# Performance work log

Measured on AMD Instinct MI355X. Metric: run time of the kernel, lower is better.

The kernel has to match this reference:

```python
import jax, jax.numpy as jnp
import numpy as np

SEQ_LEN = 720
PRED_LEN = 720
PERIOD = 24
EMB = 64
P_IN = SEQ_LEN // PERIOD            # 30
P_OUT = -(-PRED_LEN // PERIOD)      # 30 (ceil)
FREQ = EMB // 2 + 1                 # 33
DOM = (SEQ_LEN // PERIOD + 1) * 2 + 10  # 72
RATIO = PRED_LEN / SEQ_LEN          # 1.0


def _clin(z, Wr, Wi, br, bi):
    # complex nn.Linear over last dim: z @ W.T + b
    W = Wr + 1j * Wi
    b = br + 1j * bi
    return jnp.einsum('...i,oi->...o', z, W) + b


def _forward(x, freq_Wr, freq_Wi, freq_br, freq_bi, WP_W, WP_b, W_pos,
             mix1_Wr, mix1_Wi, mix1_br, mix1_bi,
             fmix_Wr, fmix_Wi, fmix_br, fmix_bi,
             proj_Wr, proj_Wi, proj_br, proj_bi,
             head_W, head_b):
    B, T, N = x.shape
    # ---- low-frequency branch ----
    low = jnp.fft.rfft(x, axis=1)[:, :DOM, :]               # [B, DOM, N] complex
    low = jnp.swapaxes(low, 1, 2)                           # [B, N, DOM]
    low = _clin(low, freq_Wr, freq_Wi, freq_br, freq_bi)    # [B, N, DOM_out]
    low = jnp.swapaxes(low, 1, 2)                           # [B, DOM_out, N]
    out_bins = PRED_LEN // 2 + 1
    low = jnp.pad(low, ((0, 0), (0, out_bins - low.shape[1]), (0, 0)))
    low_xy = jnp.fft.irfft(low, n=PRED_LEN, axis=1) * RATIO  # [B, PRED_LEN, N]

    # ---- period branch (single fixed period 24; SEQ_LEN % 24 == 0) ----
    xk = jnp.swapaxes(x, 1, 2).reshape(B, N, P_IN, PERIOD)  # unfold(size=step=24)
    xk = jnp.einsum('bnpi,oi->bnpo', xk, WP_W) + WP_b       # [B,N,P_IN,EMB]
    pf = jnp.fft.rfft(xk, axis=-1) + W_pos                  # [B,N,P_IN,FREQ] (W_pos real -> real part)
    pf = jnp.swapaxes(pf, -1, -2)                           # [B,N,FREQ,P_IN]
    o = _clin(pf, mix1_Wr, mix1_Wi, mix1_br, mix1_bi) + pf
    o = jnp.swapaxes(_clin(jnp.swapaxes(o, -1, -2), fmix_Wr, fmix_Wi, fmix_br, fmix_bi), -1, -2) + o
    o = _clin(o, proj_Wr, proj_Wi, proj_br, proj_bi)        # [B,N,FREQ,P_OUT]
    o = jnp.swapaxes(o, -1, -2)                             # [B,N,P_OUT,FREQ]
    pp = jnp.fft.irfft(o, n=EMB, axis=-1).reshape(B, N, P_OUT * EMB)
    pred = jnp.einsum('bnf,of->bno', pp, head_W) + head_b   # [B,N,PRED_LEN]
    pred = jnp.swapaxes(pred, 1, 2)                         # [B,PRED_LEN,N]
    return 0.7 * pred + 0.3 * low_xy


def setup_inputs() -> dict:
    B, N = 128, 128
    ks = jax.random.split(jax.random.key(0), 22)
    f32 = jnp.float32
    def w(k, shape, s=0.05):
        return jax.random.normal(k, shape, dtype=f32) * s
    return {
        'x': jax.random.normal(ks[0], (B, SEQ_LEN, N), dtype=f32),
        'freq_Wr': w(ks[1], (DOM, DOM)), 'freq_Wi': w(ks[2], (DOM, DOM)),
        'freq_br': w(ks[3], (DOM,)), 'freq_bi': w(ks[4], (DOM,)),
        'WP_W': w(ks[5], (EMB, PERIOD)), 'WP_b': w(ks[6], (EMB,)),
        'W_pos': jax.random.uniform(ks[7], (B, N, P_IN, FREQ), dtype=f32, minval=-0.02, maxval=0.02),
        'mix1_Wr': w(ks[8], (P_IN, P_IN)), 'mix1_Wi': w(ks[9], (P_IN, P_IN)),
        'mix1_br': w(ks[10], (P_IN,)), 'mix1_bi': w(ks[11], (P_IN,)),
        'fmix_Wr': w(ks[12], (FREQ, FREQ)), 'fmix_Wi': w(ks[13], (FREQ, FREQ)),
        'fmix_br': w(ks[14], (FREQ,)), 'fmix_bi': w(ks[15], (FREQ,)),
        'proj_Wr': w(ks[16], (P_OUT, P_IN)), 'proj_Wi': w(ks[17], (P_OUT, P_IN)),
        'proj_br': w(ks[18], (P_OUT,)), 'proj_bi': w(ks[19], (P_OUT,)),
        'head_W': w(ks[20], (PRED_LEN, P_OUT * EMB)), 'head_b': w(ks[21], (PRED_LEN,)),
    }


def reference(x, freq_Wr, freq_Wi, freq_br, freq_bi, WP_W, WP_b, W_pos,
              mix1_Wr, mix1_Wi, mix1_br, mix1_bi,
              fmix_Wr, fmix_Wi, fmix_br, fmix_bi,
              proj_Wr, proj_Wi, proj_br, proj_bi,
              head_W, head_b):
    return _forward(x, freq_Wr, freq_Wi, freq_br, freq_bi, WP_W, WP_b, W_pos,
                    mix1_Wr, mix1_Wi, mix1_br, mix1_bi,
                    fmix_Wr, fmix_Wi, fmix_br, fmix_bi,
                    proj_Wr, proj_Wi, proj_br, proj_bi,
                    head_W, head_b)
```

## Files before the change

kernel.cpp:

```cpp
#include <hip/hip_runtime.h>
#include <hip/hip_bf16.h>
#include <math.h>

#define SEQ 720
#define NCH 128
#define BATCH 128
#define BN 16384
#define DOM 72
#define PIN 30
#define POUT 30
#define FRQ 33
#define EMB 64
#define PER 24
#define KW 990
#define KP 1728
#define MT 768
#define PI_F 3.14159265358979323846f

typedef float2 cf;
typedef __attribute__((ext_vector_type(8))) short short8v;
__device__ __forceinline__ cf cmac(cf acc, cf a, cf b){
  acc.x += a.x*b.x - a.y*b.y; acc.y += a.x*b.y + a.y*b.x; return acc;
}
__device__ __forceinline__ short b2s(float f){
  __hip_bfloat16 h = __float2bfloat16(f);
  return *reinterpret_cast<short*>(&h);
}

__global__ __launch_bounds__(512) void fused_pre(
                         const float* __restrict__ WPW, const float* __restrict__ WPb,
                         const float* __restrict__ m1r, const float* __restrict__ m1i,
                         const float* __restrict__ m1br, const float* __restrict__ m1bi,
                         const float* __restrict__ fxr, const float* __restrict__ fxi,
                         const float* __restrict__ fxbr, const float* __restrict__ fxbi,
                         const float* __restrict__ pjr, const float* __restrict__ pji,
                         const float* __restrict__ pjbr, const float* __restrict__ pjbi,
                         const float* __restrict__ fqr, const float* __restrict__ fqi,
                         const float* __restrict__ x, const float* __restrict__ Wp,
                         cf* C, cf* PM, cf* M2, cf* o3b,
                         float* __restrict__ A1r, float* __restrict__ A1i,
                         __hip_bfloat16* __restrict__ Abig)
{
  __shared__ double arena_d[5900];
  char* smem = (char*)arena_d;
  int tid = threadIdx.x;
  int blk = blockIdx.x;

  if (blk < DOM){
    cf* tbl  = (cf*)(smem);
    cf* wrow = (cf*)(smem + 5760);
    int k = blk;
    for (int m=tid;m<720;m+=512){ float s,c; sincosf(-2.f*PI_F*(float)m/720.f,&s,&c); tbl[m]=make_float2(c,s); }
    for (int j=tid;j<DOM;j+=512) wrow[j]=make_float2(fqr[k*DOM+j], fqi[k*DOM+j]);
    __syncthreads();
    for (int tau=tid; tau<720; tau+=512){
      cf acc=make_float2(0.f,0.f);
      for (int j=0;j<DOM;++j) acc = cmac(acc, wrow[j], tbl[(j*tau)%720]);
      A1r[k*720+tau]=acc.x;
      A1i[k*720+tau]=acc.y;
    }
    return;
  }

  if (blk == DOM){
    cf*    e64  = (cf*)(smem + 0);
    float* sW   = (float*)(smem + 512);
    float* sWb  = (float*)(smem + 6656);
    float* sM1r = (float*)(smem + 6912);
    float* sM1i = (float*)(smem + 10512);
    float* sFxr = (float*)(smem + 14112);
    float* sFxi = (float*)(smem + 18468);
    float* sPjr = (float*)(smem + 22824);
    float* sPji = (float*)(smem + 26424);
    float* sB   = (float*)(smem + 30024);
    cf*    s_d  = (cf*)(smem + 30816);
    cf*    s_rs = (cf*)(smem + 31080);
    cf*    s_o1 = (cf*)(smem + 31320);
    cf*    s_o2 = (cf*)(smem + 39240);
    if (tid < 64){ float s,c; sincosf(2.f*PI_F*tid/64.f, &s, &c); e64[tid] = make_float2(c, s); }
    for (int i=tid; i<EMB*PER; i+=512) sW[i]=WPW[i];
    if (tid < EMB) sWb[tid]=WPb[tid];
    for (int i=tid; i<PIN*PIN; i+=512){ sM1r[i]=m1r[i]; sM1i[i]=m1i[i]; sPjr[i]=pjr[i]; sPji[i]=pji[i]; }
    for (int i=tid; i<FRQ*FRQ; i+=512){ sFxr[i]=fxr[i]; sFxi[i]=fxi[i]; }
    if (tid < PIN)  { sB[tid]      = m1br[tid]; sB[33+tid]  = m1bi[tid]; }
    if (tid < FRQ)  { sB[66+tid]   = fxbr[tid]; sB[99+tid]  = fxbi[tid]; }
    if (tid < POUT) { sB[132+tid]  = pjbr[tid]; sB[165+tid] = pjbi[tid]; }
    __syncthreads();
    for (int idx=tid; idx<FRQ*PER; idx+=512){
      int f = idx/PER, i = idx%PER;
      cf acc = make_float2(0.f,0.f);
      #pragma unroll 8
      for (int o=0;o<EMB;++o){ cf e = e64[(f*o)&63]; float w = sW[o*PER+i]; acc.x += w*e.x; acc.y -= w*e.y; }
      C[idx] = acc;
    }
    for (int f=tid; f<FRQ; f+=512){
      cf acc = make_float2(0.f,0.f);
      #pragma unroll 8
      for (int o=0;o<EMB;++o){ cf e = e64[(f*o)&63]; acc.x += sWb[o]*e.x; acc.y -= sWb[o]*e.y; }
      s_d[f]=acc;
    }
    for (int idx=tid; idx<POUT*PIN; idx+=512){
      int q = idx/PIN, pp = idx%PIN;
      cf acc = make_float2(sPjr[q*PIN+pp], sPji[q*PIN+pp]);
      #pragma unroll 6
      for (int p=0;p<PIN;++p){
        cf a = make_float2(sPjr[q*PIN+p], sPji[q*PIN+p]);
        cf b = make_float2(sM1r[p*PIN+pp], sM1i[p*PIN+pp]);
        acc = cmac(acc, a, b);
      }
      PM[idx]=acc;
    }
    for (int idx=tid; idx<FRQ*FRQ; idx+=512){
      int f = idx/FRQ, ff = idx%FRQ;
      cf v = make_float2(sFxr[idx], sFxi[idx]); if (f==ff) v.x += 1.f;
      M2[idx]=v;
    }
    for (int p=tid; p<PIN; p+=512){
      cf acc = make_float2(1.f,0.f);
      #pragma unroll 6
      for (int pp=0;pp<PIN;++pp){ acc.x += sM1r[p*PIN+pp]; acc.y += sM1i[p*PIN+pp]; }
      s_rs[p]=acc;
    }
    __syncthreads();
    for (int idx=tid; idx<FRQ*PIN; idx+=512){
      int f = idx/PIN, p = idx%PIN;
      cf v = make_float2(0.f,0.f); v = cmac(v, s_d[f], s_rs[p]);
      v.x += sB[p]; v.y += sB[33+p];
      s_o1[idx]=v;
    }
    __syncthreads();
    for (int idx=tid; idx<FRQ*PIN; idx+=512){
      int f = idx/PIN, p = idx%PIN;
      cf acc = make_float2(sB[66+f], sB[99+f]);
      #pragma unroll 4
      for (int ff=0; ff<FRQ; ++ff){
        cf m2 = make_float2(sFxr[f*FRQ+ff], sFxi[f*FRQ+ff]); if (f==ff) m2.x += 1.f;
        acc = cmac(acc, m2, s_o1[ff*PIN+p]);
      }
      s_o2[idx]=acc;
    }
    __syncthreads();
    for (int idx=tid; idx<FRQ*POUT; idx+=512){
      int f = idx/POUT, q = idx%POUT;
      cf acc = make_float2(sB[132+q], sB[165+q]);
      #pragma unroll 6
      for (int p=0;p<PIN;++p){
        cf a = make_float2(sPjr[q*PIN+p], sPji[q*PIN+p]);
        acc = cmac(acc, a, s_o2[f*PIN+p]);
      }
      o3b[f*POUT+q]=acc;
    }
    return;
  }

  if (blk < DOM + 1 + 3072){
    float (*tile)[68] = (float(*)[68])smem;
    int bb = blk - (DOM+1);
    int b = bb/24; int rem = bb%24;
    int t0 = (rem>>1)*64, n0 = (rem&1)*64;
    int r0 = tid >> 4;
    int c4 = (tid & 15)*4;
    #pragma unroll
    for (int s=0;s<2;++s){
      int r = r0 + s*32;
      int t = t0 + r;
      float4 v = make_float4(0.f,0.f,0.f,0.f);
      if (t < SEQ) v = *reinterpret_cast<const float4*>(&x[((size_t)b*SEQ + t)*NCH + n0 + c4]);
      *reinterpret_cast<float4*>(&tile[r][c4]) = v;
    }
    __syncthreads();
    int n  = tid & 63;
    int tg = tid >> 6;
    int tt = tg*8;
    if (t0 + tt < SEQ){
      short8v v;
      #pragma unroll
      for (int j=0;j<8;++j) v[j] = b2s(tile[tt+j][n]);
      *reinterpret_cast<short8v*>(Abig + (size_t)(b*NCH + n0+n)*KP + t0 + tt) = v;
    }
    return;
  }

  {
    int bb = blk - (DOM+1) - 3072;
    int lane8 = tid >> 6;
    int bn = bb*8 + lane8;
    int j = (tid & 63)*4;
    const float* src = Wp + (size_t)bn*KW;
    __hip_bfloat16* dstb = Abig + (size_t)bn*KP + SEQ;
    for (int jj = j; jj < KP-SEQ; jj += 256){
      float f0,f1,f2,f3;
      if (jj+3 < KW){
        float2 u = *reinterpret_cast<const float2*>(src+jj);
        float2 w = *reinterpret_cast<const float2*>(src+jj+2);
        f0=u.x; f1=u.y; f2=w.x; f3=w.y;
      } else {
        f0=(jj  <KW)?src[jj  ]:0.f; f1=(jj+1<KW)?src[jj+1]:0.f;
        f2=(jj+2<KW)?src[jj+2]:0.f; f3=(jj+3<KW)?src[jj+3]:0.f;
      }
      short4 v = { b2s(f0), b2s(f1), b2s(f2), b2s(f3) };
      *reinterpret_cast<short4*>(dstb + jj) = v;
    }
  }
}

__global__ __launch_bounds__(512) void p_big3(const float* __restrict__ hW,
                    const cf* __restrict__ PM, const cf* __restrict__ M2, const cf* __restrict__ o3b,
                    const cf* __restrict__ Cm,
                    const float* __restrict__ fbr, const float* __restrict__ fbi,
                    const float* __restrict__ headb,
                    const float* __restrict__ A1r, const float* __restrict__ A1i,
                    __hip_bfloat16* __restrict__ BTm, float* __restrict__ bias){
  __shared__ double smem_d[6336];
  char* smem = (char*)smem_d;
  int tid = threadIdx.x;
  cf*    e64 = (cf*)(smem + 0);
  float* shw = (float*)(smem + 512);
  cf*    sHc = (cf*)(smem + 8192);
  cf*    sV1 = (cf*)(smem + 16112);
  cf*    sPM = (cf*)(smem + 24032);
  cf*    sM2 = (cf*)(smem + 31232);
  cf*    sO3 = (cf*)(smem + 39944);
  float* red = (float*)(smem + 47864);
  float* sG  = (float*)(smem + 49912);
  cf* sC = (cf*)shw;
  cf* sV = sHc;
  int t = blockIdx.x;
  if (tid<64){ float s,c; sincosf(2.f*PI_F*tid/64.f,&s,&c); e64[tid]=make_float2(c,s); }
  if (tid<DOM){
    int m=(tid*t)%720; float s,c; sincosf(2.f*PI_F*(float)m/720.f,&s,&c);
    float sc=(tid==0)?(1.f/720.f):(2.f/720.f);
    sG[tid]=c*sc; sG[72+tid]=s*sc;
  }
  for (int i=tid;i<1920;i+=512) shw[i]=hW[(size_t)t*1920+i];
  for (int i=tid;i<POUT*PIN;i+=512) sPM[i]=PM[i];
  for (int i=tid;i<FRQ*FRQ;i+=512) sM2[i]=M2[i];
  for (int i=tid;i<FRQ*POUT;i+=512) sO3[i]=o3b[i];
  __syncthreads();
  for (int idx=tid; idx<990; idx+=512){
    int q=idx/FRQ, f=idx%FRQ;
    cf acc=make_float2(0.f,0.f);
    const float* hw = &shw[q*64];
    #pragma unroll 8
    for (int o=0;o<EMB;++o){ cf e=e64[(f*o)&63]; float w=hw[o]; acc.x+=w*e.x; acc.y+=w*e.y; }
    float s=((f==0)||(f==32))?(1.f/64.f):(2.f/64.f);
    sHc[idx]=make_float2(acc.x*s, acc.y*s);
  }
  __syncthreads();
  for (int idx=tid; idx<990; idx+=512){
    int f=idx/PIN, p=idx%PIN;
    cf acc=make_float2(0.f,0.f);
    #pragma unroll 6
    for (int q=0;q<POUT;++q) acc=cmac(acc, sHc[q*FRQ+f], sPM[q*PIN+p]);
    sV1[idx]=acc;
  }
  float part=0.f;
  for (int idx=tid; idx<990; idx+=512){
    int q=idx/FRQ, f=idx%FRQ;
    cf h=sHc[idx]; cf o=sO3[f*POUT+q];
    part += h.x*o.x - h.y*o.y;
  }
  part *= 0.7f;
  if (tid<DOM){
    int m=(tid*t)%720; float s,c; sincosf(2.f*PI_F*(float)m/720.f,&s,&c);
    float sc=(tid==0)?(1.f/720.f):(2.f/720.f);
    part += 0.3f*sc*(c*fbr[tid] - s*fbi[tid]);
  }
  for (int i=tid;i<FRQ*PER;i+=512) sC[i]=Cm[i];
  red[tid]=part; __syncthreads();
  for (int s=256;s>0;s>>=1){ if (tid<s) red[tid]+=red[tid+s]; __syncthreads(); }
  if (tid==0) bias[t] = red[0] + 0.7f*headb[t];
  __syncthreads();
  for (int idx=tid; idx<990; idx+=512){
    int ff=idx/PIN, pp=idx%PIN;
    cf acc=make_float2(0.f,0.f);
    #pragma unroll 4
    for (int f=0;f<FRQ;++f) acc=cmac(acc, sV1[f*PIN+pp], sM2[f*FRQ+ff]);
    sV[idx]=acc;
  }
  __syncthreads();
  for (int tau=tid; tau<720; tau+=512){
    int p0 = tau/PER, i0 = tau - p0*PER;
    float mper=0.f;
    #pragma unroll 4
    for (int f=0; f<FRQ; ++f){ cf v=sV[f*PIN+p0]; cf c=sC[f*PER+i0]; mper += v.x*c.x - v.y*c.y; }
    float mlow=0.f;
    #pragma unroll 8
    for (int k=0;k<DOM;++k)
      mlow += sG[k]*A1r[k*720+tau] - sG[72+k]*A1i[k*720+tau];
    BTm[(size_t)t*KP + tau] = __float2bfloat16(0.3f*mlow + 0.7f*mper);
  }
  for (int j=tid;j<KP-SEQ;j+=512){
    float v = 0.f;
    if (j < KW){ int p=j/FRQ, f=j-p*FRQ; v = 0.7f * sV[f*PIN+p].x; }
    BTm[(size_t)t*KP + SEQ + j] = __float2bfloat16(v);
  }
}

typedef __attribute__((ext_vector_type(8))) short bfrag_t;
typedef __attribute__((ext_vector_type(4))) float accf_t;
typedef __attribute__((address_space(1))) void gvoid;
typedef __attribute__((address_space(3))) void lvoid;

__device__ __forceinline__ void gload16(const void* g, void* l){
  __builtin_amdgcn_global_load_lds((gvoid*)(g), (lvoid*)(l), 16, 0, 0);
}

__global__ __launch_bounds__(256) void gemm_main(const __hip_bfloat16* __restrict__ BTm,
                                                 const __hip_bfloat16* __restrict__ Abig,
                                                 const float* __restrict__ bias,
                                                 float* __restrict__ out)
{
  __shared__ __hip_bfloat16 At[128*32];
  __shared__ __hip_bfloat16 Bt[128*32];
  int tid = threadIdx.x;
  int lane = tid & 63;
  int wv = tid >> 6;
  int wr = wv >> 1, wc = wv & 1;
  int t0 = blockIdx.y*128, bn0 = blockIdx.x*128;

  accf_t acc[4][4];
  #pragma unroll
  for (int i=0;i<4;++i)
    #pragma unroll
    for (int j=0;j<4;++j) acc[i][j] = (accf_t){0.f,0.f,0.f,0.f};

  int lin0 = tid, lin1 = 256+tid;
  int row0 = lin0>>2, ug0 = (lin0&3) ^ ((row0>>1)&3);
  int row1 = lin1>>2, ug1 = (lin1&3) ^ ((row1>>1)&3);
  const __hip_bfloat16* gA0 = BTm  + (size_t)(t0 +row0)*KP + ug0*8;
  const __hip_bfloat16* gA1 = BTm  + (size_t)(t0 +row1)*KP + ug1*8;
  const __hip_bfloat16* gB0 = Abig + (size_t)(bn0+row0)*KP + ug0*8;
  const __hip_bfloat16* gB1 = Abig + (size_t)(bn0+row1)*KP + ug1*8;
  char* lA0 = (char*)At + lin0*16; char* lA1 = (char*)At + lin1*16;
  char* lB0 = (char*)Bt + lin0*16; char* lB1 = (char*)Bt + lin1*16;

  int g = lane>>4;
  int arow = wr*64 + (lane&15);
  int brow = wc*64 + (lane&15);

  for (int ks=0; ks<KP/32; ++ks){
    int k0 = ks*32;
    gload16(gA0 + k0, lA0);
    gload16(gA1 + k0, lA1);
    gload16(gB0 + k0, lB0);
    gload16(gB1 + k0, lB1);
    __syncthreads();
    bfrag_t af[4], bb[4];
    #pragma unroll
    for (int mi=0;mi<4;++mi){
      int r = arow + mi*16;
      int uu = g ^ ((r>>1)&3);
      af[mi] = *(const bfrag_t*)((const char*)At + r*64 + uu*16);
    }
    #pragma unroll
    for (int ni=0;ni<4;++ni){
      int r = brow + ni*16;
      int uu = g ^ ((r>>1)&3);
      bb[ni] = *(const bfrag_t*)((const char*)Bt + r*64 + uu*16);
    }
    #pragma unroll
    for (int mi=0;mi<4;++mi)
      #pragma unroll
      for (int ni=0;ni<4;++ni)
        acc[mi][ni] = __builtin_amdgcn_mfma_f32_16x16x32_bf16(af[mi], bb[ni], acc[mi][ni], 0, 0, 0);
    __syncthreads();
  }

  #pragma unroll
  for (int mi=0;mi<4;++mi){
    int tbase = t0 + wr*64 + mi*16 + (lane>>4)*4;
    #pragma unroll
    for (int ni=0;ni<4;++ni){
      int col = bn0 + wc*64 + ni*16 + (lane&15);
      int b = col>>7, n = col&127;
      size_t obase = (size_t)b*(SEQ*NCH) + n;
      #pragma unroll
      for (int r=0;r<4;++r){
        int t = tbase + r;
        if (t<SEQ) out[obase + (size_t)t*NCH] = acc[mi][ni][r] + bias[t];
      }
    }
  }
}

extern "C" void kernel_launch(void* const* d_in, const int* in_sizes, int n_in,
                              void* d_out, int out_size, void* d_ws, size_t ws_size,
                              hipStream_t stream)
{
  const float* x     = (const float*)d_in[0];
  const float* fqWr  = (const float*)d_in[1];
  const float* fqWi  = (const float*)d_in[2];
  const float* fqbr  = (const float*)d_in[3];
  const float* fqbi  = (const float*)d_in[4];
  const float* WPW   = (const float*)d_in[5];
  const float* WPb   = (const float*)d_in[6];
  const float* Wpos  = (const float*)d_in[7];
  const float* m1r   = (const float*)d_in[8];
  const float* m1i   = (const float*)d_in[9];
  const float* m1br  = (const float*)d_in[10];
  const float* m1bi  = (const float*)d_in[11];
  const float* fxr   = (const float*)d_in[12];
  const float* fxi   = (const float*)d_in[13];
  const float* fxbr  = (const float*)d_in[14];
  const float* fxbi  = (const float*)d_in[15];
  const float* pjr   = (const float*)d_in[16];
  const float* pji   = (const float*)d_in[17];
  const float* pjbr  = (const float*)d_in[18];
  const float* pjbi  = (const float*)d_in[19];
  const float* headW = (const float*)d_in[20];
  const float* headb = (const float*)d_in[21];

  char* ws = (char*)d_ws;
  size_t off = 0;
  auto alloc = [&](size_t bytes)->void*{ void* p = ws + off; off += (bytes + 255) & ~(size_t)255; return p; };
  __hip_bfloat16* Abig = (__hip_bfloat16*)alloc((size_t)BN*KP*2);
  __hip_bfloat16* BTm  = (__hip_bfloat16*)alloc((size_t)MT*KP*2);
  float* A1r = (float*)alloc((size_t)DOM*720*4);
  float* A1i = (float*)alloc((size_t)DOM*720*4);
  cf* C   = (cf*)alloc((size_t)FRQ*PER*8);
  cf* PM  = (cf*)alloc((size_t)POUT*PIN*8);
  cf* M2  = (cf*)alloc((size_t)FRQ*FRQ*8);
  cf* o3b = (cf*)alloc((size_t)FRQ*POUT*8);
  float* bias = (float*)alloc((size_t)SEQ*4);

  fused_pre<<<DOM+1+3072+2048,512,0,stream>>>(WPW,WPb, m1r,m1i,m1br,m1bi, fxr,fxi,fxbr,fxbi,
                                              pjr,pji,pjbr,pjbi, fqWr,fqWi, x, Wpos,
                                              C,PM,M2,o3b, A1r,A1i, Abig);
  p_big3<<<SEQ,512,0,stream>>>(headW, PM, M2, o3b, C, fqbr, fqbi, headb, A1r, A1i, BTm, bias);
  gemm_main<<<dim3(128, 6), 256, 0, stream>>>(BTm, Abig, bias, (float*)d_out);
}
```

Baseline: 128.6 us.

## Double-buffer LDS tiles in main GEMM to overlap global loads with MFMA

Splits the shared-memory A/B tiles into two buffers and prefetches the next K-slice with direct global-to-LDS loads while computing on the current one. A manual vmcnt wait and raw s_barrier replace the __syncthreads pair, so the load latency should be hidden behind the MFMA work. This doubles LDS usage, which may reduce occupancy. It also relies on hand-placed waitcnt and scheduling barriers being correct.

```diff
diff --git a/kernel.cpp b/kernel.cpp
--- a/kernel.cpp
+++ b/kernel.cpp
@@ -311,8 +311,8 @@
                                                  const float* __restrict__ bias,
                                                  float* __restrict__ out)
 {
-  __shared__ __hip_bfloat16 At[128*32];
-  __shared__ __hip_bfloat16 Bt[128*32];
+  __shared__ __hip_bfloat16 Abuf[2][128*32];
+  __shared__ __hip_bfloat16 Bbuf[2][128*32];
   int tid = threadIdx.x;
   int lane = tid & 63;
   int wv = tid >> 6;
@@ -332,39 +332,57 @@
   const __hip_bfloat16* gA1 = BTm  + (size_t)(t0 +row1)*KP + ug1*8;
   const __hip_bfloat16* gB0 = Abig + (size_t)(bn0+row0)*KP + ug0*8;
   const __hip_bfloat16* gB1 = Abig + (size_t)(bn0+row1)*KP + ug1*8;
-  char* lA0 = (char*)At + lin0*16; char* lA1 = (char*)At + lin1*16;
-  char* lB0 = (char*)Bt + lin0*16; char* lB1 = (char*)Bt + lin1*16;
+  int off0 = lin0*16, off1 = lin1*16;
 
   int g = lane>>4;
   int arow = wr*64 + (lane&15);
   int brow = wc*64 + (lane&15);
 
-  for (int ks=0; ks<KP/32; ++ks){
-    int k0 = ks*32;
-    gload16(gA0 + k0, lA0);
-    gload16(gA1 + k0, lA1);
-    gload16(gB0 + k0, lB0);
-    gload16(gB1 + k0, lB1);
-    __syncthreads();
+  gload16(gA0, (char*)Abuf[0] + off0);
+  gload16(gA1, (char*)Abuf[0] + off1);
+  gload16(gB0, (char*)Bbuf[0] + off0);
+  gload16(gB1, (char*)Bbuf[0] + off1);
+
+  const int NKS = KP/32;
+  for (int ks=0; ks<NKS; ++ks){
+    int cur = ks & 1;
+    if (ks+1 < NKS){
+      int kn = (ks+1)*32;
+      char* an = (char*)Abuf[cur^1];
+      char* bn_ = (char*)Bbuf[cur^1];
+      gload16(gA0 + kn, an + off0);
+      gload16(gA1 + kn, an + off1);
+      gload16(gB0 + kn, bn_ + off0);
+      gload16(gB1 + kn, bn_ + off1);
+      asm volatile("s_waitcnt vmcnt(4)");
+    } else {
+      asm volatile("s_waitcnt vmcnt(0)");
+    }
+    __builtin_amdgcn_sched_barrier(0);
+    __builtin_amdgcn_s_barrier();
+    __builtin_amdgcn_sched_barrier(0);
+    const char* Ab = (const char*)Abuf[cur];
+    const char* Bb = (const char*)Bbuf[cur];
     bfrag_t af[4], bb[4];
     #pragma unroll
     for (int mi=0;mi<4;++mi){
       int r = arow + mi*16;
       int uu = g ^ ((r>>1)&3);
-      af[mi] = *(const bfrag_t*)((const char*)At + r*64 + uu*16);
+      af[mi] = *(const bfrag_t*)(Ab + r*64 + uu*16);
     }
     #pragma unroll
     for (int ni=0;ni<4;++ni){
       int r = brow + ni*16;
       int uu = g ^ ((r>>1)&3);
-      bb[ni] = *(const bfrag_t*)((const char*)Bt + r*64 + uu*16);
+      bb[ni] = *(const bfrag_t*)(Bb + r*64 + uu*16);
     }
     #pragma unroll
     for (int mi=0;mi<4;++mi)
       #pragma unroll
       for (int ni=0;ni<4;++ni)
         acc[mi][ni] = __builtin_amdgcn_mfma_f32_16x16x32_bf16(af[mi], bb[ni], acc[mi][ni], 0, 0, 0);
-    __syncthreads();
+    __builtin_amdgcn_sched_barrier(0);
+    __builtin_amdgcn_s_barrier();
   }
 
   #pragma unroll
```

Result: no change. 130.6 us (+1.5%).
